# Optimization experiments

Hardware: AMD Instinct MI355X
Metric: run time of the kernel (lower is better)

## Reference

```python
import math
import jax, jax.numpy as jnp
import numpy as np

N_WIRES = 12
N_LAYERS = 3
BATCH = 2048
DIM = 2 ** N_WIRES


def _apply_1q(psi, U, wire):
    # psi: (B, 2^n) complex; U: (2,2) or (B,2,2)
    B = psi.shape[0]
    left = 2 ** wire
    psi = psi.reshape(B, left, 2, -1)
    if U.ndim == 3:
        psi = jnp.einsum('bij,bajc->baic', U, psi)
    else:
        psi = jnp.einsum('ij,bajc->baic', U, psi)
    return psi.reshape(B, -1)


def _apply_cnot(psi, wire):
    # CNOT on (control=wire, target=wire+1), adjacent wires
    B = psi.shape[0]
    left = 2 ** wire
    psi = psi.reshape(B, left, 2, 2, -1)
    flipped = psi[:, :, 1, ::-1, :][:, :, None]   # control=1 branch, target flipped
    psi = jnp.concatenate([psi[:, :, 0:1], flipped], axis=2)
    return psi.reshape(B, -1)


def _ry(theta):
    # RY(t) = [[cos t/2, -sin t/2],[sin t/2, cos t/2]]; theta: () or (B,)
    c = jnp.cos(theta / 2)
    s = jnp.sin(theta / 2)
    U = jnp.stack([jnp.stack([c, -s], -1), jnp.stack([s, c], -1)], -2)
    return U.astype(jnp.complex64)


def _rz(theta):
    # RZ(t) = diag(e^{-it/2}, e^{it/2}); theta scalar
    em = jnp.exp(-0.5j * theta.astype(jnp.complex64))
    ep = jnp.exp(0.5j * theta.astype(jnp.complex64))
    e00 = jnp.array([[1, 0], [0, 0]], dtype=jnp.complex64)
    e11 = jnp.array([[0, 0], [0, 1]], dtype=jnp.complex64)
    return e00 * em + e11 * ep


def _measure_z(psi):
    # <Z_w> for every wire; psi: (B, 2^n)
    B = psi.shape[0]
    p = jnp.abs(psi) ** 2
    outs = []
    for w in range(N_WIRES):
        pr = p.reshape(B, 2 ** w, 2, -1)
        outs.append(pr[:, :, 0].sum((1, 2)) - pr[:, :, 1].sum((1, 2)))
    return jnp.stack(outs, axis=-1)  # (B, n_wires)


def _forward(x, W1, b1, ry_theta, rz_theta, W2, b2):
    feat = x @ W1.T + b1                      # (B, n_wires)
    angles = jnp.tanh(feat) * math.pi         # encoding angles
    B = x.shape[0]
    psi = jnp.zeros((B, DIM), dtype=jnp.complex64).at[:, 0].set(1.0)
    # data encoding: per-sample RY on each wire
    for w in range(N_WIRES):
        psi = _apply_1q(psi, _ry(angles[:, w]), w)
    # variational layers with SHARED ry/rz params (module reuse in torch code)
    Ury = _ry(ry_theta)
    Urz = _rz(rz_theta)
    for _ in range(N_LAYERS):
        for w in range(N_WIRES):
            psi = _apply_1q(psi, Ury, w)
            psi = _apply_1q(psi, Urz, w)
        for w in range(N_WIRES - 1):
            psi = _apply_cnot(psi, w)
    z = _measure_z(psi)                        # (B, n_wires) real
    return z @ W2.T + b2                       # (B, 10) logits


def setup_inputs() -> dict:
    key = jax.random.key(0)
    ks = jax.random.split(key, 7)
    return {
        'x': jax.random.normal(ks[0], (BATCH, 784), dtype=jnp.float32),
        'W1': jax.random.normal(ks[1], (N_WIRES, 784), dtype=jnp.float32) * 0.03,
        'b1': jnp.zeros((N_WIRES,), dtype=jnp.float32),
        'ry_theta': jax.random.uniform(ks[2], (), dtype=jnp.float32) * 2 * math.pi,
        'rz_theta': jax.random.uniform(ks[3], (), dtype=jnp.float32) * 2 * math.pi,
        'W2': jax.random.normal(ks[4], (10, N_WIRES), dtype=jnp.float32) * 0.2,
        'b2': jnp.zeros((10,), dtype=jnp.float32),
    }


def reference(x, W1, b1, ry_theta, rz_theta, W2, b2):
    return _forward(x, W1, b1, ry_theta, rz_theta, W2, b2)
```

## Files before the change

kernel.cpp:

```cpp
#include <hip/hip_runtime.h>
#include <math.h>

#define NW   12
#define DIM  4096
#define TPB  256

__device__ __forceinline__ float2 cmulq(float2 a, float2 b) {
    return make_float2(fmaf(a.x, b.x, -a.y * b.y), fmaf(a.x, b.y, a.y * b.x));
}

template<int CTRL>
__device__ __forceinline__ float fdpp(float v) {
    union { float f; int i; } u, w;
    u.f = v;
    w.i = __builtin_amdgcn_update_dpp(0, u.i, CTRL, 0xF, 0xF, false);
    return w.f;
}

template<int B>
__device__ __forceinline__ void ry_reg(float2* r, float c, float s) {
#pragma unroll
    for (int p = 0; p < 8; ++p) {
        const int i0 = ((p >> B) << (B + 1)) | (p & ((1 << B) - 1));
        const int i1 = i0 | (1 << B);
        const float2 a = r[i0], b = r[i1];
        r[i0].x = fmaf(-s, b.x, c * a.x);
        r[i0].y = fmaf(-s, b.y, c * a.y);
        r[i1].x = fmaf( s, a.x, c * b.x);
        r[i1].y = fmaf( s, a.y, c * b.y);
    }
}

template<int CTRL>
__device__ __forceinline__ void ry_dpp(float2* r, float c, float sp) {
#pragma unroll
    for (int k = 0; k < 16; ++k) {
        const float px = fdpp<CTRL>(r[k].x);
        const float py = fdpp<CTRL>(r[k].y);
        r[k].x = fmaf(sp, px, c * r[k].x);
        r[k].y = fmaf(sp, py, c * r[k].y);
    }
}

__global__ __launch_bounds__(TPB, 4)
void qmnist_kernel(const float* __restrict__ x,  const float* __restrict__ W1,
                   const float* __restrict__ b1, const float* __restrict__ ryp,
                   const float* __restrict__ rzp, const float* __restrict__ W2,
                   const float* __restrict__ b2, float* __restrict__ out) {
    __shared__ float2 psi[DIM];
    float* smf  = (float*)psi;
    float* wred = smf;
    float* encc = smf + 48;
    float* encs = smf + 60;
    float* zfin = smf + 72;

    const int tid  = threadIdx.x;
    const int blk  = blockIdx.x;
    const int lane = tid & 63;
    const int wave = tid >> 6;

    float acc[NW];
#pragma unroll
    for (int w = 0; w < NW; ++w) acc[w] = 0.f;
    if (tid < 196) {
        const float4 xv = ((const float4*)(x + (size_t)blk * 784))[tid];
#pragma unroll
        for (int w = 0; w < NW; ++w) {
            const float4 wv = ((const float4*)(W1 + w * 784))[tid];
            acc[w] = fmaf(xv.x, wv.x, fmaf(xv.y, wv.y, fmaf(xv.z, wv.z, xv.w * wv.w)));
        }
    }
#pragma unroll
    for (int w = 0; w < NW; ++w) {
        float v = acc[w];
        v += __shfl_down(v, 32);
        v += __shfl_down(v, 16);
        v += __shfl_down(v, 8);
        v += __shfl_down(v, 4);
        v += __shfl_down(v, 2);
        v += __shfl_down(v, 1);
        if (lane == 0) wred[wave * NW + w] = v;
    }
    __syncthreads();
    if (tid < NW) {
        float feat = wred[tid] + wred[NW + tid] + wred[2 * NW + tid] + wred[3 * NW + tid] + b1[tid];
        float a = tanhf(feat) * 3.14159265358979323846f;
        float h = 0.5f * a;
        encc[tid] = cosf(h);
        encs[tid] = sinf(h);
    }
    __syncthreads();

    float hi = 1.f;
#pragma unroll
    for (int b = 0; b < 8; ++b)
        hi *= ((tid >> b) & 1) ? encs[11 - b] : encc[11 - b];
    float2 r[16];
#pragma unroll
    for (int k = 0; k < 16; ++k) {
        float f = hi;
        f *= (k & 1) ? encs[3] : encc[3];
        f *= (k & 2) ? encs[2] : encc[2];
        f *= (k & 4) ? encs[1] : encc[1];
        f *= (k & 8) ? encs[0] : encc[0];
        r[k] = make_float2(f, 0.f);
    }

    const float ry = ryp[0], rz = rzp[0];
    const float c = cosf(0.5f * ry), s = sinf(0.5f * ry);
    const int pcT = __popc(tid);
    float2 q[5];
#pragma unroll
    for (int j = 0; j < 5; ++j) {
        const float ang = rz * (float)(pcT + j - 6);
        q[j] = make_float2(cosf(ang), sinf(ang));
    }

    const float s0p = (lane & 1)  ? s : -s;
    const float s1p = (lane & 2)  ? s : -s;
    const float s3p = (lane & 8)  ? s : -s;
    const float s5p = (lane & 32) ? s : -s;

    const int baseA = (lane & 43) | ((lane & 4) << 6) | ((lane & 16) << 5) | (wave << 10);
    const int gt    = tid ^ (tid >> 1);

    for (int layer = 0; layer < 3; ++layer) {
        __syncthreads();

        ry_reg<0>(r, c, s); ry_reg<1>(r, c, s); ry_reg<2>(r, c, s); ry_reg<3>(r, c, s);

        ry_dpp<0xB1>(r, c, s0p);
        ry_dpp<0x4E>(r, c, s1p);
        ry_dpp<0x128>(r, c, s3p);
#pragma unroll
        for (int k = 0; k < 16; ++k) {
            const float px = __shfl_xor(r[k].x, 32, 64);
            const float py = __shfl_xor(r[k].y, 32, 64);
            r[k].x = fmaf(s5p, px, c * r[k].x);
            r[k].y = fmaf(s5p, py, c * r[k].y);
        }

#pragma unroll
        for (int k = 0; k < 16; ++k)
            psi[(k << 8) | tid] = r[k];
        __syncthreads();
#pragma unroll
        for (int k = 0; k < 16; ++k)
            r[k] = psi[baseA | ((k & 1) << 2) | ((k & 2) << 3) | ((k & 4) << 4) | ((k & 8) << 4)];

        ry_reg<0>(r, c, s); ry_reg<1>(r, c, s); ry_reg<2>(r, c, s); ry_reg<3>(r, c, s);

#pragma unroll
        for (int k = 0; k < 16; ++k)
            r[k] = cmulq(r[k], q[__popc(k)]);

        __syncthreads();
#pragma unroll
        for (int k = 0; k < 16; ++k)
            psi[baseA | ((k & 1) << 2) | ((k & 2) << 3) | ((k & 4) << 4) | ((k & 8) << 4)] = r[k];
        __syncthreads();
#pragma unroll
        for (int k = 0; k < 16; ++k) {
            const int g = ((k & 1) ? (gt ^ 128) : gt) | (((k ^ (k >> 1)) & 15) << 8);
            r[k] = psi[g];
        }
    }
    __syncthreads();

    float t_total = 0.f, s3 = 0.f, s2 = 0.f, s1 = 0.f, s0 = 0.f;
#pragma unroll
    for (int k = 0; k < 16; ++k) {
        const float pp = fmaf(r[k].x, r[k].x, r[k].y * r[k].y);
        t_total += pp;
        if (k & 1) s3 += pp;
        if (k & 2) s2 += pp;
        if (k & 4) s1 += pp;
        if (k & 8) s0 += pp;
    }
    float contrib[NW];
    contrib[3] = t_total - 2.f * s3;
    contrib[2] = t_total - 2.f * s2;
    contrib[1] = t_total - 2.f * s1;
    contrib[0] = t_total - 2.f * s0;
#pragma unroll
    for (int b = 0; b < 8; ++b) {
        const int w = 11 - b;
        contrib[w] = ((tid >> b) & 1) ? -t_total : t_total;
    }
#pragma unroll
    for (int w = 0; w < NW; ++w) {
        float v = contrib[w];
        v += __shfl_down(v, 32);
        v += __shfl_down(v, 16);
        v += __shfl_down(v, 8);
        v += __shfl_down(v, 4);
        v += __shfl_down(v, 2);
        v += __shfl_down(v, 1);
        if (lane == 0) wred[wave * NW + w] = v;
    }
    __syncthreads();
    if (tid < NW)
        zfin[tid] = wred[tid] + wred[NW + tid] + wred[2 * NW + tid] + wred[3 * NW + tid];
    __syncthreads();

    if (tid < 10) {
        float o = b2[tid];
#pragma unroll
        for (int w = 0; w < NW; ++w)
            o = fmaf(zfin[w], W2[tid * NW + w], o);
        out[(size_t)blk * 10 + tid] = o;
    }
}

extern "C" void kernel_launch(void* const* d_in, const int* in_sizes, int n_in,
                              void* d_out, int out_size, void* d_ws, size_t ws_size,
                              hipStream_t stream) {
    const float* x   = (const float*)d_in[0];
    const float* W1  = (const float*)d_in[1];
    const float* b1  = (const float*)d_in[2];
    const float* ry  = (const float*)d_in[3];
    const float* rz  = (const float*)d_in[4];
    const float* W2  = (const float*)d_in[5];
    const float* b2  = (const float*)d_in[6];
    float* out = (float*)d_out;

    const int batch = in_sizes[0] / 784;
    qmnist_kernel<<<batch, TPB, 0, stream>>>(x, W1, b1, ry, rz, W2, b2, out);
}
```

Baseline: 118.6 us.

## Vectorize amplitude math with packed float2 FMAs and remap shared-memory layout

Replaces scalar float2 arithmetic with ext_vector_type(2) elementwise FMAs so the compiler can emit packed FP32 instructions for the RY rotations, DPP/shuffle mixing and RZ phase multiply. It also changes the shared-memory index permutation used for the two transposes per layer, with per-thread bases plus compile-time offsets. The new layout is meant to cut address arithmetic and LDS bank conflicts. The risk is that the new permutation must stay consistent across the write/read pairs and the CNOT gather.

```diff
diff --git a/kernel.cpp b/kernel.cpp
--- a/kernel.cpp
+++ b/kernel.cpp
@@ -5,9 +5,7 @@
 #define DIM  4096
 #define TPB  256
 
-__device__ __forceinline__ float2 cmulq(float2 a, float2 b) {
-    return make_float2(fmaf(a.x, b.x, -a.y * b.y), fmaf(a.x, b.y, a.y * b.x));
-}
+typedef float v2f __attribute__((ext_vector_type(2)));
 
 template<int CTRL>
 __device__ __forceinline__ float fdpp(float v) {
@@ -18,27 +16,23 @@
 }
 
 template<int B>
-__device__ __forceinline__ void ry_reg(float2* r, float c, float s) {
+__device__ __forceinline__ void ry_reg(v2f* r, float c, v2f vps, v2f vms) {
 #pragma unroll
     for (int p = 0; p < 8; ++p) {
         const int i0 = ((p >> B) << (B + 1)) | (p & ((1 << B) - 1));
         const int i1 = i0 | (1 << B);
-        const float2 a = r[i0], b = r[i1];
-        r[i0].x = fmaf(-s, b.x, c * a.x);
-        r[i0].y = fmaf(-s, b.y, c * a.y);
-        r[i1].x = fmaf( s, a.x, c * b.x);
-        r[i1].y = fmaf( s, a.y, c * b.y);
+        const v2f a = r[i0], b = r[i1];
+        r[i0] = __builtin_elementwise_fma(vms, b, a * c);
+        r[i1] = __builtin_elementwise_fma(vps, a, b * c);
     }
 }
 
 template<int CTRL>
-__device__ __forceinline__ void ry_dpp(float2* r, float c, float sp) {
+__device__ __forceinline__ void ry_dpp(v2f* r, float c, v2f vsp) {
 #pragma unroll
     for (int k = 0; k < 16; ++k) {
-        const float px = fdpp<CTRL>(r[k].x);
-        const float py = fdpp<CTRL>(r[k].y);
-        r[k].x = fmaf(sp, px, c * r[k].x);
-        r[k].y = fmaf(sp, py, c * r[k].y);
+        const v2f p = { fdpp<CTRL>(r[k].x), fdpp<CTRL>(r[k].y) };
+        r[k] = __builtin_elementwise_fma(vsp, p, r[k] * c);
     }
 }
 
@@ -47,7 +41,7 @@
                    const float* __restrict__ b1, const float* __restrict__ ryp,
                    const float* __restrict__ rzp, const float* __restrict__ W2,
                    const float* __restrict__ b2, float* __restrict__ out) {
-    __shared__ float2 psi[DIM];
+    __shared__ v2f psi[DIM];
     float* smf  = (float*)psi;
     float* wred = smf;
     float* encc = smf + 48;
@@ -95,7 +89,7 @@
 #pragma unroll
     for (int b = 0; b < 8; ++b)
         hi *= ((tid >> b) & 1) ? encs[11 - b] : encc[11 - b];
-    float2 r[16];
+    v2f r[16];
 #pragma unroll
     for (int k = 0; k < 16; ++k) {
         float f = hi;
@@ -103,66 +97,81 @@
         f *= (k & 2) ? encs[2] : encc[2];
         f *= (k & 4) ? encs[1] : encc[1];
         f *= (k & 8) ? encs[0] : encc[0];
-        r[k] = make_float2(f, 0.f);
+        r[k] = (v2f){ f, 0.f };
     }
 
     const float ry = ryp[0], rz = rzp[0];
     const float c = cosf(0.5f * ry), s = sinf(0.5f * ry);
+    const v2f vps = {  s,  s };
+    const v2f vms = { -s, -s };
     const int pcT = __popc(tid);
-    float2 q[5];
+    v2f qv[5], qp[5];
 #pragma unroll
     for (int j = 0; j < 5; ++j) {
         const float ang = rz * (float)(pcT + j - 6);
-        q[j] = make_float2(cosf(ang), sinf(ang));
-    }
-
-    const float s0p = (lane & 1)  ? s : -s;
-    const float s1p = (lane & 2)  ? s : -s;
-    const float s3p = (lane & 8)  ? s : -s;
-    const float s5p = (lane & 32) ? s : -s;
-
-    const int baseA = (lane & 43) | ((lane & 4) << 6) | ((lane & 16) << 5) | (wave << 10);
-    const int gt    = tid ^ (tid >> 1);
+        const float qc = cosf(ang), qs = sinf(ang);
+        qv[j] = (v2f){  qc, qs };
+        qp[j] = (v2f){ -qs, qc };
+    }
+
+    const v2f vs0 = (lane & 1)  ? vps : vms;
+    const v2f vs1 = (lane & 2)  ? vps : vms;
+    const v2f vs3 = (lane & 8)  ? vps : vms;
+    const v2f vs5 = (lane & 32) ? vps : vms;
+
+    const int t0 = tid & 1,        t1 = (tid >> 1) & 1, t2 = (tid >> 2) & 1,
+              t3 = (tid >> 3) & 1, t4 = (tid >> 4) & 1, t5 = (tid >> 5) & 1;
+    const int wbaseA = (tid & 3) | (t3 << 2) | (t5 << 3) | (t2 << 4) | (t4 << 5) | (tid & 192);
+    const int rbaseA = (tid & 3) | (t3 << 2) | (t5 << 3) | (t2 << 8) | (t4 << 9) | ((tid & 192) << 4);
+    const int wbaseC = (tid & 3) | (t3 << 2) | (t5 << 3) | (t2 << 4) | (t4 << 5) | ((tid & 192) << 4);
+    const int gt = tid ^ (tid >> 1);
+    const int rbaseC0 = (gt & 1) | (((gt >> 1) & 1) << 1) | (((gt >> 3) & 1) << 2) |
+                        (((gt >> 5) & 1) << 3) | (((gt >> 2) & 1) << 6) |
+                        (((gt >> 4) & 1) << 7) | (((gt >> 6) & 1) << 8) | (((gt >> 7) & 1) << 9);
+    const int rbaseC1 = rbaseC0 ^ 512;
 
     for (int layer = 0; layer < 3; ++layer) {
         __syncthreads();
 
-        ry_reg<0>(r, c, s); ry_reg<1>(r, c, s); ry_reg<2>(r, c, s); ry_reg<3>(r, c, s);
-
-        ry_dpp<0xB1>(r, c, s0p);
-        ry_dpp<0x4E>(r, c, s1p);
-        ry_dpp<0x128>(r, c, s3p);
+        ry_reg<0>(r, c, vps, vms); ry_reg<1>(r, c, vps, vms);
+        ry_reg<2>(r, c, vps, vms); ry_reg<3>(r, c, vps, vms);
+
+        ry_dpp<0xB1>(r, c, vs0);
+        ry_dpp<0x4E>(r, c, vs1);
+        ry_dpp<0x128>(r, c, vs3);
 #pragma unroll
         for (int k = 0; k < 16; ++k) {
-            const float px = __shfl_xor(r[k].x, 32, 64);
-            const float py = __shfl_xor(r[k].y, 32, 64);
-            r[k].x = fmaf(s5p, px, c * r[k].x);
-            r[k].y = fmaf(s5p, py, c * r[k].y);
+            const v2f p = { __shfl_xor(r[k].x, 32, 64), __shfl_xor(r[k].y, 32, 64) };
+            r[k] = __builtin_elementwise_fma(vs5, p, r[k] * c);
         }
 
 #pragma unroll
         for (int k = 0; k < 16; ++k)
-            psi[(k << 8) | tid] = r[k];
+            psi[wbaseA + (k << 8)] = r[k];
         __syncthreads();
 #pragma unroll
         for (int k = 0; k < 16; ++k)
-            r[k] = psi[baseA | ((k & 1) << 2) | ((k & 2) << 3) | ((k & 4) << 4) | ((k & 8) << 4)];
-
-        ry_reg<0>(r, c, s); ry_reg<1>(r, c, s); ry_reg<2>(r, c, s); ry_reg<3>(r, c, s);
-
+            r[k] = psi[rbaseA + (k << 4)];
+
+        ry_reg<0>(r, c, vps, vms); ry_reg<1>(r, c, vps, vms);
+        ry_reg<2>(r, c, vps, vms); ry_reg<3>(r, c, vps, vms);
+
+#pragma unroll
+        for (int k = 0; k < 16; ++k) {
+            const int j = __popc(k);
+            r[k] = __builtin_elementwise_fma((v2f){ r[k].y, r[k].y }, qp[j], qv[j] * r[k].x);
+        }
+
+        __syncthreads();
 #pragma unroll
         for (int k = 0; k < 16; ++k)
-            r[k] = cmulq(r[k], q[__popc(k)]);
-
-        __syncthreads();
-#pragma unroll
-        for (int k = 0; k < 16; ++k)
-            psi[baseA | ((k & 1) << 2) | ((k & 2) << 3) | ((k & 4) << 4) | ((k & 8) << 4)] = r[k];
+            psi[wbaseC + (k << 6)] = r[k];
         __syncthreads();
 #pragma unroll
         for (int k = 0; k < 16; ++k) {
-            const int g = ((k & 1) ? (gt ^ 128) : gt) | (((k ^ (k >> 1)) & 15) << 8);
-            r[k] = psi[g];
+            const int gk   = (k ^ (k >> 1)) & 15;
+            const int immC = ((gk & 3) << 4) | ((gk & 12) << 8);
+            r[k] = psi[((k & 1) ? rbaseC1 : rbaseC0) + immC];
         }
     }
     __syncthreads();
```

New measurement: 123.3 us. 4.0% more time.
